# Kernel optimization log

Hardware: AMD Instinct MI355X
Metric: run time of the kernel (lower is better)

The kernel has to match this reference:

```python
import jax, jax.numpy as jnp
import numpy as np

B, C, CB, WIDTH = 16, 256, 64, 32
F = CB * WIDTH  # lstm_features = 2048


def setup_inputs() -> dict:
    key = jax.random.key(0)
    ks = jax.random.split(key, 14)
    s = 0.02  # ~1/sqrt(F), torch default uniform(-1/sqrt(h), 1/sqrt(h)) scale
    return {
        "x": jax.random.normal(ks[0], (B, C, WIDTH, WIDTH), jnp.float32),
        "w_in": jax.random.normal(ks[1], (CB, C), jnp.float32) * s,
        "b_in": jax.random.normal(ks[2], (CB,), jnp.float32) * s,
        "W_ih0": jax.random.normal(ks[3], (4 * F, F), jnp.float32) * s,
        "W_hh0": jax.random.normal(ks[4], (4 * F, F), jnp.float32) * s,
        "b_ih0": jax.random.normal(ks[5], (4 * F,), jnp.float32) * s,
        "b_hh0": jax.random.normal(ks[6], (4 * F,), jnp.float32) * s,
        "W_ih1": jax.random.normal(ks[7], (4 * F, F), jnp.float32) * s,
        "W_hh1": jax.random.normal(ks[8], (4 * F, F), jnp.float32) * s,
        "b_ih1": jax.random.normal(ks[9], (4 * F,), jnp.float32) * s,
        "b_hh1": jax.random.normal(ks[10], (4 * F,), jnp.float32) * s,
        "w_out": jax.random.normal(ks[11], (C, CB), jnp.float32) * s,
        "b_out": jax.random.normal(ks[12], (C,), jnp.float32) * s,
    }


def _lstm_cell(x_t, h, c, W_ih, W_hh, b_ih, b_hh):
    # torch nn.LSTM gate order: i, f, g, o
    g = x_t @ W_ih.T + h @ W_hh.T + (b_ih + b_hh)
    i, f, gg, o = jnp.split(g, 4, axis=-1)
    c_n = jax.nn.sigmoid(f) * c + jax.nn.sigmoid(i) * jnp.tanh(gg)
    h_n = jax.nn.sigmoid(o) * jnp.tanh(c_n)
    return h_n, c_n


def reference(x, w_in, b_in, W_ih0, W_hh0, b_ih0, b_hh0,
              W_ih1, W_hh1, b_ih1, b_hh1, w_out, b_out):
    Bn, Cn, H, W = x.shape
    # 1x1 conv bottleneck in -> [B, Cb, H, W]
    bn = jnp.einsum('bchw,oc->bohw', x, w_in) + b_in[None, :, None, None]
    Cb = bn.shape[1]
    Ff = W * Cb
    # rows as sequence: [H, B, W*Cb], feature index = w*Cb + c
    seq = bn.transpose(2, 0, 3, 1).reshape(H, Bn, Ff)

    def step(states, x_t):
        h0, c0, h1, c1 = states
        h0, c0 = _lstm_cell(x_t, h0, c0, W_ih0, W_hh0, b_ih0, b_hh0)
        h1, c1 = _lstm_cell(h0, h1, c1, W_ih1, W_hh1, b_ih1, b_hh1)
        return (h0, c0, h1, c1), h1

    z = jnp.zeros((Bn, Ff), x.dtype)
    states, outs = jax.lax.scan(step, (z, z, z, z), seq)
    y0 = outs[-1]  # out[-1]: first generated row

    def gen(carry, _):
        st, y = carry
        st, y_n = step(st, y)
        return (st, y_n), y_n

    _, gen_outs = jax.lax.scan(gen, (states, y0), None, length=W - 1)
    seq_out = jnp.concatenate([y0[None], gen_outs], axis=0)  # [W, B, F]

    # un-flatten back to spatial: [B, S=W, W, Cb] then 1x1 conv out -> [B, C, S, W]
    spatial = seq_out.transpose(1, 0, 2).reshape(Bn, W, W, Cb)
    y = jnp.einsum('bswc,oc->bosw', spatial, w_out) + b_out[None, :, None, None]
    # stitch generated rows below input along height dim
    return jnp.concatenate([x, y], axis=2)
```

## Files before the change

### kernel.cpp

```cpp
#include <hip/hip_runtime.h>
#include <hip/hip_bf16.h>

typedef unsigned short u16;
typedef unsigned char uchar;
typedef unsigned long long u64;
typedef float f32x4 __attribute__((ext_vector_type(4)));
typedef int i8v __attribute__((ext_vector_type(8)));

#define FDIM 2048
#define NBLK 256
#define NCELL 126

__device__ __forceinline__ u16 f2b(float x) {
    __hip_bfloat16 h = __float2bfloat16(x);
    return __builtin_bit_cast(u16, h);
}
__device__ __forceinline__ float b2f(u16 u) {
    __hip_bfloat16 h = __builtin_bit_cast(__hip_bfloat16, u);
    return __bfloat162float(h);
}
__device__ __forceinline__ float sigm(float x) { return 1.0f / (1.0f + __expf(-x)); }
__device__ __forceinline__ float tanh_f(float x) { return 1.0f - 2.0f / (__expf(2.0f * x) + 1.0f); }

__device__ __forceinline__ unsigned f2fp8(float x) {
    unsigned u = __builtin_bit_cast(unsigned, x);
    unsigned s = (u >> 24) & 0x80u;
    unsigned mag = u & 0x7fffffffu;
    if (mag >= 0x43E80000u) return s | 0x7Eu;
    int e = (int)(mag >> 23) - 127;
    if (e >= -6) {
        unsigned m = mag + 0x7FFFFu + ((mag >> 20) & 1u);
        unsigned e8 = (m >> 23) - 127 + 7;
        unsigned m3 = (m >> 20) & 7u;
        if (e8 >= 16u) return s | 0x7Eu;
        return s | (e8 << 3) | m3;
    }
    float ax = __builtin_bit_cast(float, mag);
    int d = (int)__builtin_rintf(ax * 512.0f);
    return s | (unsigned)d;
}

__device__ __forceinline__ unsigned q_e2m1(float v) {
    unsigned s = (v < 0.f) ? 8u : 0u;
    float a = fabsf(v);
    unsigned q;
    if (a < 0.25f) q = 0;
    else if (a < 0.75f) q = 1;
    else if (a < 1.25f) q = 2;
    else if (a < 1.75f) q = 3;
    else if (a < 2.5f)  q = 4;
    else if (a < 3.5f)  q = 5;
    else if (a < 5.0f)  q = 6;
    else q = 7;
    return s | q;
}

__global__ __launch_bounds__(256) void k_pack4(const float* __restrict__ W0, const float* __restrict__ W1,
                                               const float* __restrict__ W2, const float* __restrict__ W3,
                                               uchar* __restrict__ Wp4, uchar* __restrict__ scl) {
    __shared__ float lw[32][132];
    int idx = blockIdx.x;
    int kt = idx & 15, mat = (idx >> 4) & 3, bl = idx >> 6;
    const float* src = mat == 0 ? W0 : mat == 1 ? W1 : mat == 2 ? W2 : W3;
    int tid = threadIdx.x;
    for (int i = tid; i < 32 * 32; i += 256) {
        int r = i >> 5, c4 = i & 31;
        const float* p = src + (size_t)((r >> 3) * 2048 + bl * 8 + (r & 7)) * 2048 + kt * 128 + c4 * 4;
        float4 v = *(const float4*)p;
        lw[r][c4 * 4 + 0] = v.x; lw[r][c4 * 4 + 1] = v.y;
        lw[r][c4 * 4 + 2] = v.z; lw[r][c4 * 4 + 3] = v.w;
    }
    __syncthreads();
    if (tid < 128) {
        int gp = tid >> 6, lane = tid & 63;
        int r = (2 * gp + ((lane & 15) >> 3)) * 8 + (lane & 7);
        int k0 = (lane >> 4) * 32;
        float mx = 0.f;
#pragma unroll
        for (int e = 0; e < 32; ++e) mx = fmaxf(mx, fabsf(lw[r][k0 + e]));
        int ee = -127;
        if (mx > 0.f) {
            ee = (int)ceilf(log2f(mx * (1.0f / 6.0f)));
            if (ee < -127) ee = -127;
            if (ee > 127) ee = 127;
        }
        float inv = exp2f((float)(-ee));
        unsigned wd[4];
#pragma unroll
        for (int d = 0; d < 4; ++d) {
            unsigned acc = 0;
#pragma unroll
            for (int bi = 0; bi < 4; ++bi) {
                float v0 = lw[r][k0 + d * 8 + 2 * bi] * inv;
                float v1 = lw[r][k0 + d * 8 + 2 * bi + 1] * inv;
                acc |= (q_e2m1(v0) << (bi * 8)) | (q_e2m1(v1) << (bi * 8 + 4));
            }
            wd[d] = acc;
        }
        size_t wo = (size_t)bl * 131072 + (((size_t)(mat * 2 + gp) * 16 + (size_t)kt) * 64 + lane) * 16;
        *(uint4*)(Wp4 + wo) = make_uint4(wd[0], wd[1], wd[2], wd[3]);
        scl[(((size_t)bl * 4 + mat) * 2 + gp) * 1024 + (size_t)lane * 16 + kt] = (uchar)(ee + 127);
    }
}

__global__ void k_bias(const float* __restrict__ bi0, const float* __restrict__ bh0,
                       const float* __restrict__ bi1, const float* __restrict__ bh1,
                       float* __restrict__ bias0, float* __restrict__ bias1) {
    int i = blockIdx.x * blockDim.x + threadIdx.x;
    if (i < 4 * FDIM) {
        bias0[i] = bi0[i] + bh0[i];
        bias1[i] = bi1[i] + bh1[i];
    }
}

__global__ __launch_bounds__(256) void k_seqprep(const float* __restrict__ x,
                                                 const float* __restrict__ w_in,
                                                 const float* __restrict__ b_in,
                                                 uchar* __restrict__ seqb) {
    int h = blockIdx.x >> 4, b = blockIdx.x & 15;
    __shared__ float xs[256][32];
    __shared__ float wl[64][257];
    int tid = threadIdx.x;
    for (int i = tid; i < 256 * 32; i += 256) {
        int c = i >> 5, w = i & 31;
        xs[c][w] = x[(((size_t)b * 256 + c) * 32 + h) * 32 + w];
    }
    for (int i = tid; i < 64 * 256; i += 256) {
        int cb = i >> 8, c = i & 255;
        wl[cb][c] = w_in[i];
    }
    __syncthreads();
    int w = (tid * 8) >> 6, cb0 = (tid * 8) & 63;
    float acc[8];
#pragma unroll
    for (int j = 0; j < 8; ++j) acc[j] = b_in[cb0 + j];
    for (int c = 0; c < 256; ++c) {
        float xv = xs[c][w];
#pragma unroll
        for (int j = 0; j < 8; ++j) acc[j] += xv * wl[cb0 + j][c];
    }
    unsigned lo = 0, hi2 = 0;
#pragma unroll
    for (int j = 0; j < 4; ++j) lo |= f2fp8(acc[j] * 4.0f) << (j * 8);
#pragma unroll
    for (int j = 0; j < 4; ++j) hi2 |= f2fp8(acc[4 + j] * 4.0f) << (j * 8);
    int kt = tid >> 4, kq = (tid >> 2) & 3, e0 = (tid & 3) * 8;
    uchar* dst = seqb + (size_t)h * 32768 + (size_t)kt * 2048 + (size_t)(b + 16 * kq) * 32 + e0;
    *(uint2*)dst = make_uint2(lo, hi2);
}

__global__ __launch_bounds__(576, 1) void k_lstm(const uchar* __restrict__ Wp4,
                                                 const uchar* __restrict__ scl,
                                                 const float* __restrict__ bias0,
                                                 const float* __restrict__ bias1,
                                                 const uchar* __restrict__ seqb,
                                                 uchar* __restrict__ H0, uchar* __restrict__ H1,
                                                 u16* __restrict__ seqout,
                                                 unsigned* __restrict__ tags) {
    __shared__ uchar wlds[131072];
    __shared__ float gbuf[2][8][16][20];
    __shared__ u64 hs_st[16];
    __shared__ unsigned flagLDS;
    const int tid = threadIdx.x, lane = tid & 63, w = tid >> 6;
    const int gp = w & 1, m = (w >> 1) & 1, kh = w >> 2;
    const int bl = blockIdx.x;
    const size_t BF = (size_t)16 * FDIM;

    {
        const uchar* src = Wp4 + (size_t)bl * 131072;
        for (int i = tid; i < 8192; i += 576)
            *(uint4*)(wlds + (size_t)i * 16) = *(const uint4*)(src + (size_t)i * 16);
    }
    uint4 scl0, scl1;
    if (w < 8) {
        scl0 = *(const uint4*)(scl + (((size_t)bl * 4 + m) * 2 + gp) * 1024 + (size_t)lane * 16);
        scl1 = *(const uint4*)(scl + (((size_t)bl * 4 + 2 + m) * 2 + gp) * 1024 + (size_t)lane * 16);
    }

    float bw0[2][4], bw1[2][4];
    float cs0[2] = {0.f, 0.f}, cs1[2] = {0.f, 0.f};
    if (w == 7) {
        const int f0 = (lane & 3) * 2;
#pragma unroll
        for (int i = 0; i < 2; ++i) {
            int col = bl * 8 + f0 + i;
#pragma unroll
            for (int g = 0; g < 4; ++g) {
                bw0[i][g] = bias0[g * FDIM + col];
                bw1[i][g] = bias1[g * FDIM + col];
            }
        }
    }
    if (tid == 0) flagLDS = 0;
    __syncthreads();

    const int b16 = lane & 15, kq = lane >> 4;
    for (int c = 0; c < NCELL; ++c) {
        const int s = c >> 1, isL1 = c & 1, par = c & 1;
        const uchar* xsrc = isL1 ? (H0 + (size_t)(s + 1) * BF)
                          : (s < 32 ? (seqb + (size_t)s * BF) : (H1 + (size_t)s * BF));
        const uchar* hsrc = isL1 ? (H1 + (size_t)s * BF) : (H0 + (size_t)s * BF);
        const bool staticX = (!isL1 && s < 32);

        if (w == 8) {
            if (c >= 1) {
                const unsigned* trow = tags + (size_t)(c - 1) * 2048;
                for (;;) {
                    unsigned v0 = __hip_atomic_load(trow + (size_t)lane * 8,
                                                    __ATOMIC_RELAXED, __HIP_MEMORY_SCOPE_AGENT);
                    unsigned v1 = __hip_atomic_load(trow + (size_t)(lane + 64) * 8,
                                                    __ATOMIC_RELAXED, __HIP_MEMORY_SCOPE_AGENT);
                    unsigned v2 = __hip_atomic_load(trow + (size_t)(lane + 128) * 8,
                                                    __ATOMIC_RELAXED, __HIP_MEMORY_SCOPE_AGENT);
                    unsigned v3 = __hip_atomic_load(trow + (size_t)(lane + 192) * 8,
                                                    __ATOMIC_RELAXED, __HIP_MEMORY_SCOPE_AGENT);
                    if ((v0 & v1 & v2 & v3) == 1u) break;
                    __builtin_amdgcn_s_sleep(1);
                }
                if (lane == 0)
                    __hip_atomic_store(&flagLDS, (unsigned)c,
                                       __ATOMIC_RELAXED, __HIP_MEMORY_SCOPE_WORKGROUP);
            }
        } else {
            const uchar* asrc = m ? hsrc : xsrc;
            unsigned need = m ? ((c >= 2) ? (unsigned)(c - 1) : 0u)
                             : (staticX ? 0u : (unsigned)c);
            if (need)
                while (__hip_atomic_load(&flagLDS, __ATOMIC_RELAXED,
                                         __HIP_MEMORY_SCOPE_WORKGROUP) < need)
                    __builtin_amdgcn_s_sleep(1);
            asm volatile("" ::: "memory");

            const uchar* ap = asrc + (size_t)lane * 32;
            uint4 A[8][2];
#pragma unroll
            for (int t = 0; t < 8; ++t) {
                A[t][0] = *(const uint4*)(ap + (size_t)(kh * 8 + t) * 2048);
                A[t][1] = *(const uint4*)(ap + (size_t)(kh * 8 + t) * 2048 + 16);
            }
            const uchar* bp = wlds + (size_t)((isL1 * 2 + m) * 2 + gp) * 16384 + lane * 16;
            uint4 sv = isL1 ? scl1 : scl0;
            unsigned sw0 = kh ? sv.z : sv.x;
            unsigned sw1 = kh ? sv.w : sv.y;

            f32x4 acc0 = {0.f, 0.f, 0.f, 0.f}, acc1 = {0.f, 0.f, 0.f, 0.f};
#define MF(T, SW, J)                                                                   \
            {                                                                          \
                uint4 alo = A[T][0], ahi = A[T][1];                                    \
                uint4 bb = *(const uint4*)(bp + (kh * 8 + (T)) * 1024);                \
                i8v av = {(int)alo.x, (int)alo.y, (int)alo.z, (int)alo.w,              \
                          (int)ahi.x, (int)ahi.y, (int)ahi.z, (int)ahi.w};             \
                i8v bv = {(int)bb.x, (int)bb.y, (int)bb.z, (int)bb.w, 0, 0, 0, 0};     \
                if ((T) & 1)                                                           \
                    acc1 = __builtin_amdgcn_mfma_scale_f32_16x16x128_f8f6f4(           \
                        av, bv, acc1, 0, 4, 0, 127, J, (int)(SW));                     \
                else                                                                   \
                    acc0 = __builtin_amdgcn_mfma_scale_f32_16x16x128_f8f6f4(           \
                        av, bv, acc0, 0, 4, 0, 127, J, (int)(SW));                     \
            }
            MF(0, sw0, 0); MF(1, sw0, 1); MF(2, sw0, 2); MF(3, sw0, 3);
            MF(4, sw1, 0); MF(5, sw1, 1); MF(6, sw1, 2); MF(7, sw1, 3);
#undef MF
            f32x4 acc = acc0 + acc1;
#pragma unroll
            for (int i = 0; i < 4; ++i) gbuf[par][w][kq * 4 + i][b16] = acc[i];
        }
        __syncthreads();

        if (w == 7) {
            const int b = lane >> 2, f0 = (lane & 3) * 2;
            u16 hb2 = 0;
            float hnv[2];
#pragma unroll
            for (int i = 0; i < 2; ++i) {
                const int f = f0 + i;
                float gv[4];
#pragma unroll
                for (int g = 0; g < 4; ++g) {
                    int gpp = g >> 1, jl = ((g & 1) << 3) | f;
                    gv[g] = (gbuf[par][gpp][b][jl] + gbuf[par][gpp + 2][b][jl]
                           + gbuf[par][gpp + 4][b][jl] + gbuf[par][gpp + 6][b][jl]) * 0.25f
                           + (isL1 ? bw1[i][g] : bw0[i][g]);
                }
                float co = isL1 ? cs1[i] : cs0[i];
                float cn = sigm(gv[1]) * co + sigm(gv[0]) * tanh_f(gv[2]);
                float hn = sigm(gv[3]) * tanh_f(cn);
                if (isL1) cs1[i] = cn; else cs0[i] = cn;
                hb2 |= (u16)(f2fp8(hn * 4.0f) << (8 * i));
                hnv[i] = hn;
            }
            *(u16*)((uchar*)&hs_st[b] + f0) = hb2;
            asm volatile("s_waitcnt lgkmcnt(0)" ::: "memory");
            if (lane < 16) {
                uchar* hdst = (isL1 ? H1 : H0) + (size_t)(s + 1) * BF;
                size_t o = (size_t)(bl >> 4) * 2048 + (size_t)((bl >> 2) & 3) * 512
                         + (size_t)(bl & 3) * 8 + (size_t)lane * 32;
                __hip_atomic_store((u64*)(hdst + o), hs_st[lane],
                                   __ATOMIC_RELAXED, __HIP_MEMORY_SCOPE_AGENT);
            }
            asm volatile("s_waitcnt vmcnt(0)" ::: "memory");
            if (lane == 0)
                __hip_atomic_store(tags + (size_t)c * 2048 + (size_t)bl * 8, 1u,
                                   __ATOMIC_RELAXED, __HIP_MEMORY_SCOPE_AGENT);
            if (isL1 && s >= 31) {
                unsigned pk = (unsigned)f2b(hnv[0]) | ((unsigned)f2b(hnv[1]) << 16);
                *(unsigned*)(seqout + (size_t)(s - 31) * BF + (size_t)b * FDIM + bl * 8 + f0) = pk;
            }
        }
    }
}

__global__ void k_copyx(const float* __restrict__ x, float* __restrict__ out) {
    size_t n = (size_t)4096 * 256;
    size_t stride = (size_t)gridDim.x * blockDim.x;
    for (size_t i = (size_t)blockIdx.x * blockDim.x + threadIdx.x; i < n; i += stride) {
        size_t bc = i >> 8, r = i & 255;
        ((float4*)out)[bc * 512 + r] = ((const float4*)x)[i];
    }
}

__global__ __launch_bounds__(256) void k_convout(const u16* __restrict__ seqout,
                                                 const float* __restrict__ w_out,
                                                 const float* __restrict__ b_out,
                                                 float* __restrict__ out) {
    int s = blockIdx.x >> 4, b = blockIdx.x & 15;
    __shared__ float srow[2048];
    int tid = threadIdx.x;
    for (int i = tid; i < 2048; i += 256) srow[i] = b2f(seqout[((size_t)s * 16 + b) * FDIM + i]);
    __syncthreads();
    int o = tid;
    float bo = b_out[o];
    float wreg[64];
#pragma unroll
    for (int cb = 0; cb < 64; ++cb) wreg[cb] = w_out[o * 64 + cb];
    for (int w4 = 0; w4 < 8; ++w4) {
        float ac0 = bo, ac1 = bo, ac2 = bo, ac3 = bo;
#pragma unroll
        for (int cb = 0; cb < 64; ++cb) {
            float wv = wreg[cb];
            ac0 += srow[(w4 * 4 + 0) * 64 + cb] * wv;
            ac1 += srow[(w4 * 4 + 1) * 64 + cb] * wv;
            ac2 += srow[(w4 * 4 + 2) * 64 + cb] * wv;
            ac3 += srow[(w4 * 4 + 3) * 64 + cb] * wv;
        }
        float4 v; v.x = ac0; v.y = ac1; v.z = ac2; v.w = ac3;
        *(float4*)&out[(((size_t)b * 256 + o) * 64 + 32 + s) * 32 + w4 * 4] = v;
    }
}

extern "C" void kernel_launch(void* const* d_in, const int* in_sizes, int n_in,
                              void* d_out, int out_size, void* d_ws, size_t ws_size,
                              hipStream_t stream) {
    const float* x    = (const float*)d_in[0];
    const float* w_in = (const float*)d_in[1];
    const float* b_in = (const float*)d_in[2];
    const float* Wih0 = (const float*)d_in[3];
    const float* Whh0 = (const float*)d_in[4];
    const float* bih0 = (const float*)d_in[5];
    const float* bhh0 = (const float*)d_in[6];
    const float* Wih1 = (const float*)d_in[7];
    const float* Whh1 = (const float*)d_in[8];
    const float* bih1 = (const float*)d_in[9];
    const float* bhh1 = (const float*)d_in[10];
    const float* wout = (const float*)d_in[11];
    const float* bout = (const float*)d_in[12];
    float* out = (float*)d_out;
    char* ws = (char*)d_ws;
    const size_t BF = (size_t)16 * FDIM;

    uchar* Wp4 = (uchar*)ws;
    size_t off = (size_t)NBLK * 131072;
    uchar* scl = (uchar*)(ws + off); off += (size_t)NBLK * 4 * 2 * 1024;
    float* bias0 = (float*)(ws + off); off += 4 * FDIM * 4;
    float* bias1 = (float*)(ws + off); off += 4 * FDIM * 4;
    uchar* seqb = (uchar*)(ws + off); off += (size_t)32 * BF;
    u16* seqout = (u16*)(ws + off); off += (size_t)32 * BF * 2;
    uchar* H0 = (uchar*)(ws + off); off += (size_t)64 * BF;
    uchar* H1 = (uchar*)(ws + off); off += (size_t)64 * BF;
    off = (off + 127) & ~(size_t)127;
    unsigned* tags = (unsigned*)(ws + off); size_t tagoff = off;
    off += (size_t)NCELL * 2048 * 4;

    hipMemsetAsync(H0, 0, BF, stream);
    hipMemsetAsync(H1, 0, BF, stream);
    hipMemsetAsync(ws + tagoff, 0, off - tagoff, stream);

    k_pack4<<<256 * 4 * 16, 256, 0, stream>>>(Wih0, Whh0, Wih1, Whh1, Wp4, scl);
    k_bias<<<32, 256, 0, stream>>>(bih0, bhh0, bih1, bhh1, bias0, bias1);
    k_seqprep<<<512, 256, 0, stream>>>(x, w_in, b_in, seqb);
    k_lstm<<<NBLK, 576, 0, stream>>>(Wp4, scl, bias0, bias1, seqb, H0, H1, seqout, tags);
    k_copyx<<<2048, 256, 0, stream>>>(x, out);
    k_convout<<<512, 256, 0, stream>>>(seqout, wout, bout, out);
}
```

Measured before the change: 651.7 us.

## Split blocks by LSTM layer to pipeline layer 0 and layer 1 concurrently

Before, every persistent block computed both LSTM layers in strict alternation: 126 serialized cells, each ending in a grid-wide tag barrier. Now half the blocks own layer 0 and half own layer 1, each covering 16 feature columns. The layers are wavefront-pipelined over 63 steps with separate tag arrays and per-layer LDS flags, so a layer-1 step can overlap the next layer-0 step. Each block's MFMA work and epilogue double (two B tiles per wave, two epilogue waves). The cross-layer dependency tracking is more intricate, which raises the risk of deadlock or ordering bugs.

Measured after the change: 620.5 us. 4.8% less time.

```diff
diff --git a/kernel.cpp b/kernel.cpp
--- a/kernel.cpp
+++ b/kernel.cpp
@@ -9,7 +9,8 @@
 
 #define FDIM 2048
 #define NBLK 256
-#define NCELL 126
+#define NSTEP 63
+#define SLOT 32768
 
 __device__ __forceinline__ u16 f2b(float x) {
     __hip_bfloat16 h = __float2bfloat16(x);
@@ -58,23 +59,24 @@
 __global__ __launch_bounds__(256) void k_pack4(const float* __restrict__ W0, const float* __restrict__ W1,
                                                const float* __restrict__ W2, const float* __restrict__ W3,
                                                uchar* __restrict__ Wp4, uchar* __restrict__ scl) {
-    __shared__ float lw[32][132];
+    __shared__ float lw[64][132];
     int idx = blockIdx.x;
-    int kt = idx & 15, mat = (idx >> 4) & 3, bl = idx >> 6;
-    const float* src = mat == 0 ? W0 : mat == 1 ? W1 : mat == 2 ? W2 : W3;
+    int kt = idx & 15, m = (idx >> 4) & 1, gb = idx >> 5;
+    int fam = gb >> 7, blf = gb & 127;
+    const float* src = (fam == 0) ? (m == 0 ? W0 : W1) : (m == 0 ? W2 : W3);
     int tid = threadIdx.x;
-    for (int i = tid; i < 32 * 32; i += 256) {
+    for (int i = tid; i < 64 * 32; i += 256) {
         int r = i >> 5, c4 = i & 31;
-        const float* p = src + (size_t)((r >> 3) * 2048 + bl * 8 + (r & 7)) * 2048 + kt * 128 + c4 * 4;
+        const float* p = src + (size_t)((r >> 4) * 2048 + blf * 16 + (r & 15)) * 2048 + kt * 128 + c4 * 4;
         float4 v = *(const float4*)p;
         lw[r][c4 * 4 + 0] = v.x; lw[r][c4 * 4 + 1] = v.y;
         lw[r][c4 * 4 + 2] = v.z; lw[r][c4 * 4 + 3] = v.w;
     }
     __syncthreads();
-    if (tid < 128) {
-        int gp = tid >> 6, lane = tid & 63;
-        int r = (2 * gp + ((lane & 15) >> 3)) * 8 + (lane & 7);
-        int k0 = (lane >> 4) * 32;
+    {
+        int jt = tid >> 6, l = tid & 63;
+        int r = jt * 16 + (l & 15);
+        int k0 = (l >> 4) * 32;
         float mx = 0.f;
 #pragma unroll
         for (int e = 0; e < 32; ++e) mx = fmaxf(mx, fabsf(lw[r][k0 + e]));
@@ -97,9 +99,9 @@
             }
             wd[d] = acc;
         }
-        size_t wo = (size_t)bl * 131072 + (((size_t)(mat * 2 + gp) * 16 + (size_t)kt) * 64 + lane) * 16;
+        size_t wo = (size_t)gb * 131072 + (size_t)((m * 4 + jt) * 16 + kt) * 1024 + (size_t)l * 16;
         *(uint4*)(Wp4 + wo) = make_uint4(wd[0], wd[1], wd[2], wd[3]);
-        scl[(((size_t)bl * 4 + mat) * 2 + gp) * 1024 + (size_t)lane * 16 + kt] = (uchar)(ee + 127);
+        scl[(size_t)gb * 8192 + (size_t)((m * 4 + jt) * 64 + l) * 16 + kt] = (uchar)(ee + 127);
     }
 }
 
@@ -145,7 +147,7 @@
 #pragma unroll
     for (int j = 0; j < 4; ++j) hi2 |= f2fp8(acc[4 + j] * 4.0f) << (j * 8);
     int kt = tid >> 4, kq = (tid >> 2) & 3, e0 = (tid & 3) * 8;
-    uchar* dst = seqb + (size_t)h * 32768 + (size_t)kt * 2048 + (size_t)(b + 16 * kq) * 32 + e0;
+    uchar* dst = seqb + (size_t)h * SLOT + (size_t)kt * 2048 + (size_t)(b + 16 * kq) * 32 + e0;
     *(uint2*)dst = make_uint2(lo, hi2);
 }
 
@@ -156,80 +158,94 @@
                                                  const uchar* __restrict__ seqb,
                                                  uchar* __restrict__ H0, uchar* __restrict__ H1,
                                                  u16* __restrict__ seqout,
-                                                 unsigned* __restrict__ tags) {
+                                                 unsigned* __restrict__ tags0,
+                                                 unsigned* __restrict__ tags1) {
     __shared__ uchar wlds[131072];
-    __shared__ float gbuf[2][8][16][20];
-    __shared__ u64 hs_st[16];
-    __shared__ unsigned flagLDS;
+    __shared__ float gbuf[4][4][16][16];
+    __shared__ u64 hs_st[16][2];
+    __shared__ unsigned flag0LDS, flag1LDS;
     const int tid = threadIdx.x, lane = tid & 63, w = tid >> 6;
-    const int gp = w & 1, m = (w >> 1) & 1, kh = w >> 2;
+    const int jp = w & 1, kh = (w >> 1) & 1, m = w >> 2;
     const int bl = blockIdx.x;
-    const size_t BF = (size_t)16 * FDIM;
+    const int fam = bl >> 7, blf = bl & 127;
 
     {
         const uchar* src = Wp4 + (size_t)bl * 131072;
         for (int i = tid; i < 8192; i += 576)
             *(uint4*)(wlds + (size_t)i * 16) = *(const uint4*)(src + (size_t)i * 16);
     }
-    uint4 scl0, scl1;
+    unsigned sw00 = 0, sw01 = 0, sw10 = 0, sw11 = 0;
     if (w < 8) {
-        scl0 = *(const uint4*)(scl + (((size_t)bl * 4 + m) * 2 + gp) * 1024 + (size_t)lane * 16);
-        scl1 = *(const uint4*)(scl + (((size_t)bl * 4 + 2 + m) * 2 + gp) * 1024 + (size_t)lane * 16);
-    }
-
-    float bw0[2][4], bw1[2][4];
-    float cs0[2] = {0.f, 0.f}, cs1[2] = {0.f, 0.f};
-    if (w == 7) {
-        const int f0 = (lane & 3) * 2;
+        const uchar* sbase = scl + (size_t)bl * 8192 + (size_t)((m * 4 + jp * 2) * 64 + lane) * 16;
+        uint4 s0 = *(const uint4*)(sbase);
+        uint4 s1 = *(const uint4*)(sbase + 1024);
+        sw00 = kh ? s0.z : s0.x; sw01 = kh ? s0.w : s0.y;
+        sw10 = kh ? s1.z : s1.x; sw11 = kh ? s1.w : s1.y;
+    }
+    float bw[2][4];
+    float cs[2] = {0.f, 0.f};
+    const int wvoff = (w == 7) ? 8 : 0;
+    if (w >= 6) {
+        const int flb = (lane & 3) * 2;
+        const float* barr = fam ? bias1 : bias0;
 #pragma unroll
         for (int i = 0; i < 2; ++i) {
-            int col = bl * 8 + f0 + i;
-#pragma unroll
-            for (int g = 0; g < 4; ++g) {
-                bw0[i][g] = bias0[g * FDIM + col];
-                bw1[i][g] = bias1[g * FDIM + col];
-            }
-        }
-    }
-    if (tid == 0) flagLDS = 0;
+            int col = blf * 16 + wvoff + flb + i;
+#pragma unroll
+            for (int g = 0; g < 4; ++g) bw[i][g] = barr[g * FDIM + col];
+        }
+    }
+    if (tid == 0) { flag0LDS = 0; flag1LDS = 0; }
     __syncthreads();
 
+    unsigned f0 = 0, f1 = 0;
     const int b16 = lane & 15, kq = lane >> 4;
-    for (int c = 0; c < NCELL; ++c) {
-        const int s = c >> 1, isL1 = c & 1, par = c & 1;
-        const uchar* xsrc = isL1 ? (H0 + (size_t)(s + 1) * BF)
-                          : (s < 32 ? (seqb + (size_t)s * BF) : (H1 + (size_t)s * BF));
-        const uchar* hsrc = isL1 ? (H1 + (size_t)s * BF) : (H0 + (size_t)s * BF);
-        const bool staticX = (!isL1 && s < 32);
-
+
+    for (int s = 0; s < NSTEP; ++s) {
         if (w == 8) {
-            if (c >= 1) {
-                const unsigned* trow = tags + (size_t)(c - 1) * 2048;
-                for (;;) {
-                    unsigned v0 = __hip_atomic_load(trow + (size_t)lane * 8,
-                                                    __ATOMIC_RELAXED, __HIP_MEMORY_SCOPE_AGENT);
-                    unsigned v1 = __hip_atomic_load(trow + (size_t)(lane + 64) * 8,
-                                                    __ATOMIC_RELAXED, __HIP_MEMORY_SCOPE_AGENT);
-                    unsigned v2 = __hip_atomic_load(trow + (size_t)(lane + 128) * 8,
-                                                    __ATOMIC_RELAXED, __HIP_MEMORY_SCOPE_AGENT);
-                    unsigned v3 = __hip_atomic_load(trow + (size_t)(lane + 192) * 8,
-                                                    __ATOMIC_RELAXED, __HIP_MEMORY_SCOPE_AGENT);
-                    if ((v0 & v1 & v2 & v3) == 1u) break;
+            int t0 = fam ? (s + 1) : s;
+            int t1 = fam ? s : ((s >= 32) ? s : 0);
+#define ADV(F, TGT, TB, FL)                                                            \
+            while ((int)F < (TGT)) {                                                   \
+                const unsigned* trow = (TB) + (size_t)F * 2048;                        \
+                for (;;) {                                                             \
+                    unsigned v0 = __hip_atomic_load(trow + (size_t)lane * 8,           \
+                                      __ATOMIC_RELAXED, __HIP_MEMORY_SCOPE_AGENT);     \
+                    unsigned v1 = __hip_atomic_load(trow + (size_t)(lane + 64) * 8,    \
+                                      __ATOMIC_RELAXED, __HIP_MEMORY_SCOPE_AGENT);     \
+                    unsigned v2 = __hip_atomic_load(trow + (size_t)(lane + 128) * 8,   \
+                                      __ATOMIC_RELAXED, __HIP_MEMORY_SCOPE_AGENT);     \
+                    unsigned v3 = __hip_atomic_load(trow + (size_t)(lane + 192) * 8,   \
+                                      __ATOMIC_RELAXED, __HIP_MEMORY_SCOPE_AGENT);     \
+                    if ((v0 & v1 & v2 & v3) == 1u) break;                              \
+                    __builtin_amdgcn_s_sleep(1);                                       \
+                }                                                                      \
+                ++F;                                                                   \
+                if (lane == 0)                                                         \
+                    __hip_atomic_store(&(FL), F, __ATOMIC_RELAXED,                     \
+                                       __HIP_MEMORY_SCOPE_WORKGROUP);                  \
+            }
+            if (fam == 0) { ADV(f0, t0, tags0, flag0LDS) ADV(f1, t1, tags1, flag1LDS) }
+            else          { ADV(f1, t1, tags1, flag1LDS) ADV(f0, t0, tags0, flag0LDS) }
+#undef ADV
+        } else {
+            unsigned need0 = 0, need1 = 0;
+            if (fam == 0) { if (m) need0 = (unsigned)s; else need1 = (s >= 32) ? (unsigned)s : 0u; }
+            else          { if (m) need1 = (unsigned)s; else need0 = (unsigned)(s + 1); }
+            if (need0)
+                while (__hip_atomic_load(&flag0LDS, __ATOMIC_RELAXED,
+                                         __HIP_MEMORY_SCOPE_WORKGROUP) < need0)
                     __builtin_amdgcn_s_sleep(1);
-                }
-                if (lane == 0)
-                    __hip_atomic_store(&flagLDS, (unsigned)c,
-                                       __ATOMIC_RELAXED, __HIP_MEMORY_SCOPE_WORKGROUP);
-            }
-        } else {
-            const uchar* asrc = m ? hsrc : xsrc;
-            unsigned need = m ? ((c >= 2) ? (unsigned)(c - 1) : 0u)
-                             : (staticX ? 0u : (unsigned)c);
-            if (need)
-                while (__hip_atomic_load(&flagLDS, __ATOMIC_RELAXED,
-                                         __HIP_MEMORY_SCOPE_WORKGROUP) < need)
+            if (need1)
+                while (__hip_atomic_load(&flag1LDS, __ATOMIC_RELAXED,
+                                         __HIP_MEMORY_SCOPE_WORKGROUP) < need1)
                     __builtin_amdgcn_s_sleep(1);
             asm volatile("" ::: "memory");
+
+            const uchar* xsrc = fam ? (H0 + (size_t)(s + 1) * SLOT)
+                              : (s < 32 ? seqb + (size_t)s * SLOT : H1 + (size_t)s * SLOT);
+            const uchar* hsrc = fam ? (H1 + (size_t)s * SLOT) : (H0 + (size_t)s * SLOT);
+            const uchar* asrc = m ? hsrc : xsrc;
 
             const uchar* ap = asrc + (size_t)lane * 32;
             uint4 A[8][2];
@@ -238,73 +254,96 @@
                 A[t][0] = *(const uint4*)(ap + (size_t)(kh * 8 + t) * 2048);
                 A[t][1] = *(const uint4*)(ap + (size_t)(kh * 8 + t) * 2048 + 16);
             }
-            const uchar* bp = wlds + (size_t)((isL1 * 2 + m) * 2 + gp) * 16384 + lane * 16;
-            uint4 sv = isL1 ? scl1 : scl0;
-            unsigned sw0 = kh ? sv.z : sv.x;
-            unsigned sw1 = kh ? sv.w : sv.y;
-
-            f32x4 acc0 = {0.f, 0.f, 0.f, 0.f}, acc1 = {0.f, 0.f, 0.f, 0.f};
-#define MF(T, SW, J)                                                                   \
+            const uchar* bp0 = wlds + (size_t)((m * 4 + jp * 2) * 16 + kh * 8) * 1024 + lane * 16;
+            const uchar* bp1 = bp0 + 16384;
+
+            f32x4 aA0 = {0.f,0.f,0.f,0.f}, aA1 = {0.f,0.f,0.f,0.f};
+            f32x4 aB0 = {0.f,0.f,0.f,0.f}, aB1 = {0.f,0.f,0.f,0.f};
+#define MF(T)                                                                          \
             {                                                                          \
                 uint4 alo = A[T][0], ahi = A[T][1];                                    \
-                uint4 bb = *(const uint4*)(bp + (kh * 8 + (T)) * 1024);                \
                 i8v av = {(int)alo.x, (int)alo.y, (int)alo.z, (int)alo.w,              \
                           (int)ahi.x, (int)ahi.y, (int)ahi.z, (int)ahi.w};             \
-                i8v bv = {(int)bb.x, (int)bb.y, (int)bb.z, (int)bb.w, 0, 0, 0, 0};     \
-                if ((T) & 1)                                                           \
-                    acc1 = __builtin_amdgcn_mfma_scale_f32_16x16x128_f8f6f4(           \
-                        av, bv, acc1, 0, 4, 0, 127, J, (int)(SW));                     \
-                else                                                                   \
-                    acc0 = __builtin_amdgcn_mfma_scale_f32_16x16x128_f8f6f4(           \
-                        av, bv, acc0, 0, 4, 0, 127, J, (int)(SW));                     \
-            }
-            MF(0, sw0, 0); MF(1, sw0, 1); MF(2, sw0, 2); MF(3, sw0, 3);
-            MF(4, sw1, 0); MF(5, sw1, 1); MF(6, sw1, 2); MF(7, sw1, 3);
+                uint4 b0 = *(const uint4*)(bp0 + (T) * 1024);                          \
+                i8v bv0 = {(int)b0.x, (int)b0.y, (int)b0.z, (int)b0.w, 0, 0, 0, 0};    \
+                uint4 b1 = *(const uint4*)(bp1 + (T) * 1024);                          \
+                i8v bv1 = {(int)b1.x, (int)b1.y, (int)b1.z, (int)b1.w, 0, 0, 0, 0};    \
+                if ((T) & 1) {                                                         \
+                    aA1 = __builtin_amdgcn_mfma_scale_f32_16x16x128_f8f6f4(            \
+                        av, bv0, aA1, 0, 4, 0, 127, (T) & 3,                           \
+                        (int)((T) < 4 ? sw00 : sw01));                                 \
+                    aB1 = __builtin_amdgcn_mfma_scale_f32_16x16x128_f8f6f4(            \
+                        av, bv1, aB1, 0, 4, 0, 127, (T) & 3,                           \
+                        (int)((T) < 4 ? sw10 : sw11));                                 \
+                } else {                                                               \
+                    aA0 = __builtin_amdgcn_mfma_scale_f32_16x16x128_f8f6f4(            \
+                        av, bv0, aA0, 0, 4, 0, 127, (T) & 3,                           \
+                        (int)((T) < 4 ? sw00 : sw01));                                 \
+                    aB0 = __builtin_amdgcn_mfma_scale_f32_16x16x128_f8f6f4(            \
+                        av, bv1, aB0, 0, 4, 0, 127, (T) & 3,                           \
+                        (int)((T) < 4 ? sw10 : sw11));                                 \
+                }                                                                      \
+            }
+            MF(0) MF(1) MF(2) MF(3) MF(4) MF(5) MF(6) MF(7)
 #undef MF
-            f32x4 acc = acc0 + acc1;
-#pragma unroll
-            for (int i = 0; i < 4; ++i) gbuf[par][w][kq * 4 + i][b16] = acc[i];
+            f32x4 rA = aA0 + aA1, rB = aB0 + aB1;
+            const int slot = m * 2 + kh;
+#pragma unroll
+            for (int i = 0; i < 4; ++i) {
+                gbuf[jp * 2 + 0][slot][kq * 4 + i][b16] = rA[i];
+                gbuf[jp * 2 + 1][slot][kq * 4 + i][b16] = rB[i];
+            }
         }
         __syncthreads();
 
-        if (w == 7) {
-            const int b = lane >> 2, f0 = (lane & 3) * 2;
+        float gsum[2][4];
+        if (w >= 6) {
+            const int b = lane >> 2, flb = (lane & 3) * 2;
+#pragma unroll
+            for (int i = 0; i < 2; ++i) {
+                const int f = wvoff + flb + i;
+#pragma unroll
+                for (int g = 0; g < 4; ++g)
+                    gsum[i][g] = gbuf[g][0][b][f] + gbuf[g][1][b][f]
+                               + gbuf[g][2][b][f] + gbuf[g][3][b][f];
+            }
+        }
+        __syncthreads();
+
+        if (w >= 6) {
+            const int b = lane >> 2, flb = (lane & 3) * 2;
             u16 hb2 = 0;
             float hnv[2];
 #pragma unroll
             for (int i = 0; i < 2; ++i) {
-                const int f = f0 + i;
                 float gv[4];
 #pragma unroll
-                for (int g = 0; g < 4; ++g) {
-                    int gpp = g >> 1, jl = ((g & 1) << 3) | f;
-                    gv[g] = (gbuf[par][gpp][b][jl] + gbuf[par][gpp + 2][b][jl]
-                           + gbuf[par][gpp + 4][b][jl] + gbuf[par][gpp + 6][b][jl]) * 0.25f
-                           + (isL1 ? bw1[i][g] : bw0[i][g]);
-                }
-                float co = isL1 ? cs1[i] : cs0[i];
-                float cn = sigm(gv[1]) * co + sigm(gv[0]) * tanh_f(gv[2]);
+                for (int g = 0; g < 4; ++g) gv[g] = gsum[i][g] * 0.25f + bw[i][g];
+                float cn = sigm(gv[1]) * cs[i] + sigm(gv[0]) * tanh_f(gv[2]);
                 float hn = sigm(gv[3]) * tanh_f(cn);
-                if (isL1) cs1[i] = cn; else cs0[i] = cn;
+                cs[i] = cn;
                 hb2 |= (u16)(f2fp8(hn * 4.0f) << (8 * i));
                 hnv[i] = hn;
             }
-            *(u16*)((uchar*)&hs_st[b] + f0) = hb2;
+            const int wv = wvoff >> 3;
+            *(u16*)((uchar*)&hs_st[b][wv] + flb) = hb2;
             asm volatile("s_waitcnt lgkmcnt(0)" ::: "memory");
+            uchar* out = (fam ? H1 : H0) + (size_t)(s + 1) * SLOT;
             if (lane < 16) {
-                uchar* hdst = (isL1 ? H1 : H0) + (size_t)(s + 1) * BF;
-                size_t o = (size_t)(bl >> 4) * 2048 + (size_t)((bl >> 2) & 3) * 512
-                         + (size_t)(bl & 3) * 8 + (size_t)lane * 32;
-                __hip_atomic_store((u64*)(hdst + o), hs_st[lane],
+                const int kt0 = blf >> 3, sub = (blf & 7) >> 1, byte0 = (blf & 1) * 16;
+                size_t o = (size_t)kt0 * 2048 + (size_t)(lane + 16 * sub) * 32 + byte0 + wvoff;
+                __hip_atomic_store((u64*)(out + o), hs_st[lane][wv],
                                    __ATOMIC_RELAXED, __HIP_MEMORY_SCOPE_AGENT);
             }
             asm volatile("s_waitcnt vmcnt(0)" ::: "memory");
-            if (lane == 0)
-                __hip_atomic_store(tags + (size_t)c * 2048 + (size_t)bl * 8, 1u,
-                                   __ATOMIC_RELAXED, __HIP_MEMORY_SCOPE_AGENT);
-            if (isL1 && s >= 31) {
+            if (lane == 0) {
+                unsigned* tg = (fam ? tags1 : tags0) + (size_t)s * 2048 + (size_t)(blf * 2 + wv) * 8;
+                __hip_atomic_store(tg, 1u, __ATOMIC_RELAXED, __HIP_MEMORY_SCOPE_AGENT);
+            }
+            if (fam && s >= 31) {
                 unsigned pk = (unsigned)f2b(hnv[0]) | ((unsigned)f2b(hnv[1]) << 16);
-                *(unsigned*)(seqout + (size_t)(s - 31) * BF + (size_t)b * FDIM + bl * 8 + f0) = pk;
+                *(unsigned*)(seqout + (size_t)(s - 31) * 16 * FDIM
+                             + (size_t)b * FDIM + blf * 16 + wvoff + flb) = pk;
             }
         }
     }
@@ -370,25 +409,27 @@
 
     uchar* Wp4 = (uchar*)ws;
     size_t off = (size_t)NBLK * 131072;
-    uchar* scl = (uchar*)(ws + off); off += (size_t)NBLK * 4 * 2 * 1024;
+    uchar* scl = (uchar*)(ws + off); off += (size_t)NBLK * 8192;
     float* bias0 = (float*)(ws + off); off += 4 * FDIM * 4;
     float* bias1 = (float*)(ws + off); off += 4 * FDIM * 4;
-    uchar* seqb = (uchar*)(ws + off); off += (size_t)32 * BF;
+    uchar* seqb = (uchar*)(ws + off); off += (size_t)32 * SLOT;
     u16* seqout = (u16*)(ws + off); off += (size_t)32 * BF * 2;
-    uchar* H0 = (uchar*)(ws + off); off += (size_t)64 * BF;
-    uchar* H1 = (uchar*)(ws + off); off += (size_t)64 * BF;
+    uchar* H0 = (uchar*)(ws + off); off += (size_t)64 * SLOT;
+    uchar* H1 = (uchar*)(ws + off); off += (size_t)64 * SLOT;
     off = (off + 127) & ~(size_t)127;
-    unsigned* tags = (unsigned*)(ws + off); size_t tagoff = off;
-    off += (size_t)NCELL * 2048 * 4;
-
-    hipMemsetAsync(H0, 0, BF, stream);
-    hipMemsetAsync(H1, 0, BF, stream);
+    unsigned* tags0 = (unsigned*)(ws + off); size_t tagoff = off;
+    off += (size_t)NSTEP * 2048 * 4;
+    unsigned* tags1 = (unsigned*)(ws + off);
+    off += (size_t)NSTEP * 2048 * 4;
+
+    hipMemsetAsync(H0, 0, SLOT, stream);
+    hipMemsetAsync(H1, 0, SLOT, stream);
     hipMemsetAsync(ws + tagoff, 0, off - tagoff, stream);
 
-    k_pack4<<<256 * 4 * 16, 256, 0, stream>>>(Wih0, Whh0, Wih1, Whh1, Wp4, scl);
+    k_pack4<<<8192, 256, 0, stream>>>(Wih0, Whh0, Wih1, Whh1, Wp4, scl);
     k_bias<<<32, 256, 0, stream>>>(bih0, bhh0, bih1, bhh1, bias0, bias1);
     k_seqprep<<<512, 256, 0, stream>>>(x, w_in, b_in, seqb);
-    k_lstm<<<NBLK, 576, 0, stream>>>(Wp4, scl, bias0, bias1, seqb, H0, H1, seqout, tags);
+    k_lstm<<<NBLK, 576, 0, stream>>>(Wp4, scl, bias0, bias1, seqb, H0, H1, seqout, tags0, tags1);
     k_copyx<<<2048, 256, 0, stream>>>(x, out);
     k_convout<<<512, 256, 0, stream>>>(seqout, wout, bout, out);
 }
```
